# Optimization experiments

Hardware: AMD Instinct MI355X
Metric: run time of the kernel (lower is better)

## Reference

```python
import jax, jax.numpy as jnp
import numpy as np
import math

NUM_HEADS = 16
HEAD_DIM = 64
EMBED = NUM_HEADS * HEAD_DIM  # 1024
T_FEAT = 128


def setup_inputs() -> dict:
    key = jax.random.key(0)
    ks = jax.random.split(key, 9)
    B, S = 4, 2048
    x = jax.random.normal(ks[0], (B, S, EMBED), dtype=jnp.float32)
    time_enc = jax.random.normal(ks[1], (B, T_FEAT), dtype=jnp.float32)
    s = 1.0 / math.sqrt(EMBED)
    Wq = jax.random.normal(ks[2], (EMBED, EMBED), dtype=jnp.float32) * s
    Wk = jax.random.normal(ks[3], (EMBED, EMBED), dtype=jnp.float32) * s
    Wv = jax.random.normal(ks[4], (EMBED, EMBED), dtype=jnp.float32) * s
    Wo = jax.random.normal(ks[5], (EMBED, EMBED), dtype=jnp.float32) * s
    bo = jnp.zeros((EMBED,), dtype=jnp.float32)
    Wt = jax.random.normal(ks[6], (T_FEAT, NUM_HEADS), dtype=jnp.float32) * (1.0 / math.sqrt(T_FEAT))
    bt = jnp.zeros((NUM_HEADS,), dtype=jnp.float32)
    return {"x": x, "time_enc": time_enc, "Wq": Wq, "Wk": Wk, "Wv": Wv,
            "Wo": Wo, "bo": bo, "Wt": Wt, "bt": bt}


def reference(x, time_enc, Wq, Wk, Wv, Wo, bo, Wt, bt):
    B, S, E = x.shape
    H, D = NUM_HEADS, HEAD_DIM
    scale = 1.0 / math.sqrt(D)
    # projections (no bias on q/k/v, bias on out)
    q = (x @ Wq).reshape(B, S, H, D).transpose(0, 2, 1, 3)  # [B,H,S,D]
    k = (x @ Wk).reshape(B, S, H, D).transpose(0, 2, 1, 3)
    v = (x @ Wv).reshape(B, S, H, D).transpose(0, 2, 1, 3)
    scores = jnp.einsum('bhqd,bhkd->bhqk', q, k) * scale
    # time-dependent per-head weighting (softmax over heads)
    time_weights = jax.nn.softmax(time_enc @ Wt + bt)  # [B,H]
    scores = scores * time_weights.reshape(B, H, 1, 1)
    attn = jax.nn.softmax(scores, axis=-1)
    out = jnp.einsum('bhqk,bhkd->bhqd', attn, v)
    out = out.transpose(0, 2, 1, 3).reshape(B, S, E)
    return out @ Wo + bo
```

## Files before the change

kernel.cpp:

```cpp
#include <hip/hip_runtime.h>
#include <cstdint>
#include <cstddef>

#define EMB   1024
#define NH    16
#define HD    64
#define SEQ   2048
#define NB    4
#define MROWS 8192

typedef short short8 __attribute__((ext_vector_type(8)));
typedef float floatx4 __attribute__((ext_vector_type(4)));

__device__ __forceinline__ unsigned short f2bf(float f) {
  return (unsigned short)((__float_as_uint(f) + 0x8000u) >> 16);
}

__device__ __forceinline__ void load16_lds(const unsigned short* g, unsigned short* l) {
  __builtin_amdgcn_global_load_lds((const __attribute__((address_space(1))) void*)g,
                                   (__attribute__((address_space(3))) void*)l, 16, 0, 0);
}

__global__ void time_weights_kernel(const float* __restrict__ te, const float* __restrict__ Wt,
                                    const float* __restrict__ bt, float* __restrict__ tw) {
  int t = threadIdx.x;
  int b = t >> 4, h = t & 15;
  float acc = bt[h];
  for (int i = 0; i < 128; i++) acc += te[b * 128 + i] * Wt[i * 16 + h];
  float m = acc;
  for (int off = 1; off < 16; off <<= 1) m = fmaxf(m, __shfl_xor(m, off, 16));
  float e = __expf(acc - m);
  float s = e;
  for (int off = 1; off < 16; off <<= 1) s += __shfl_xor(s, off, 16);
  tw[t] = (e / s) * 0.125f * 1.4426950408889634f;
}

__global__ void convert_x_kernel(const float4* __restrict__ x, unsigned short* __restrict__ out) {
  int i = blockIdx.x * blockDim.x + threadIdx.x;
  float4 v = x[i];
  unsigned int u0 = __float_as_uint(v.x) + 0x8000u, u1 = __float_as_uint(v.y) + 0x8000u;
  unsigned int u2 = __float_as_uint(v.z) + 0x8000u, u3 = __float_as_uint(v.w) + 0x8000u;
  uint2 p;
  p.x = (u0 >> 16) | (u1 & 0xffff0000u);
  p.y = (u2 >> 16) | (u3 & 0xffff0000u);
  *(uint2*)&out[(size_t)i * 4] = p;
}

__global__ void transpose_convert4_kernel(const float* __restrict__ Wq, const float* __restrict__ Wk,
                                          const float* __restrict__ Wv, const float* __restrict__ Wo,
                                          unsigned short* __restrict__ wqkvt, unsigned short* __restrict__ wot) {
  __shared__ float tile[32][33];
  int z = blockIdx.z;
  const float* W = (z == 0) ? Wq : (z == 1) ? Wk : (z == 2) ? Wv : Wo;
  unsigned short* out = (z < 3) ? (wqkvt + (size_t)z * EMB * EMB) : wot;
  int k0 = blockIdx.x * 32;
  int n0 = blockIdx.y * 32;
  int tx = threadIdx.x;
  int ty = threadIdx.y;
#pragma unroll
  for (int i = 0; i < 4; i++) {
    int k = ty + i * 8;
    tile[k][tx] = W[(size_t)(k0 + k) * EMB + n0 + tx];
  }
  __syncthreads();
#pragma unroll
  for (int i = 0; i < 4; i++) {
    int n = ty + i * 8;
    out[(size_t)(n0 + n) * EMB + k0 + tx] = f2bf(tile[tx][n]);
  }
}

template <int EPI>
__global__ __launch_bounds__(256) void gemm_kernel(
    const unsigned short* __restrict__ A, const unsigned short* __restrict__ Bt,
    unsigned short* __restrict__ qo, unsigned short* __restrict__ ko, unsigned short* __restrict__ vto,
    float* __restrict__ outf, const float* __restrict__ bias, const float* __restrict__ tw) {
  __shared__ unsigned short As[128 * 64];
  __shared__ unsigned short Bs[128 * 64];

  int tid = threadIdx.x;
  int lane = tid & 63, wid = tid >> 6;
  int quad = lane >> 4, l16 = lane & 15;
  int wm = wid >> 1, wn = wid & 1;
  int m0 = blockIdx.y * 128, n0 = blockIdx.x * 128;

  const unsigned short* gA[4];
  const unsigned short* gB[4];
  unsigned short* lA[4];
  unsigned short* lB[4];
#pragma unroll
  for (int c = 0; c < 4; c++) {
    int row = wid * 32 + c * 8 + (lane >> 3);
    int gcol = ((lane & 7) ^ (row & 7)) * 8;
    gA[c] = A + (size_t)(m0 + row) * 1024 + gcol;
    gB[c] = Bt + (size_t)(n0 + row) * 1024 + gcol;
    lA[c] = &As[(wid * 32 + c * 8) * 64];
    lB[c] = &Bs[(wid * 32 + c * 8) * 64];
  }

  int aoff[2];
#pragma unroll
  for (int kk = 0; kk < 2; kk++) aoff[kk] = (((kk * 4 + quad) ^ (l16 & 7)) * 8);

  floatx4 acc[4][4];
#pragma unroll
  for (int mi = 0; mi < 4; mi++)
#pragma unroll
    for (int ni = 0; ni < 4; ni++)
#pragma unroll
      for (int r = 0; r < 4; r++) acc[mi][ni][r] = 0.f;

  for (int k0 = 0; k0 < 1024; k0 += 64) {
    __syncthreads();
#pragma unroll
    for (int c = 0; c < 4; c++) {
      load16_lds(gA[c] + k0, lA[c]);
      load16_lds(gB[c] + k0, lB[c]);
    }
    asm volatile("s_waitcnt vmcnt(0) lgkmcnt(0)" ::: "memory");
    __syncthreads();

#pragma unroll
    for (int kk = 0; kk < 2; kk++) {
      short8 a_frag[4], b_frag[4];
#pragma unroll
      for (int mi = 0; mi < 4; mi++)
        a_frag[mi] = *(const short8*)&As[(wm * 64 + mi * 16 + l16) * 64 + aoff[kk]];
#pragma unroll
      for (int ni = 0; ni < 4; ni++)
        b_frag[ni] = *(const short8*)&Bs[(wn * 64 + ni * 16 + l16) * 64 + aoff[kk]];
#pragma unroll
      for (int mi = 0; mi < 4; mi++)
#pragma unroll
        for (int ni = 0; ni < 4; ni++)
          acc[mi][ni] = __builtin_amdgcn_mfma_f32_16x16x32_bf16(a_frag[mi], b_frag[ni], acc[mi][ni], 0, 0, 0);
    }
  }

#pragma unroll
  for (int mi = 0; mi < 4; mi++)
#pragma unroll
    for (int ni = 0; ni < 4; ni++)
#pragma unroll
      for (int r = 0; r < 4; r++) {
        int m = m0 + wm * 64 + mi * 16 + quad * 4 + r;
        int n = n0 + wn * 64 + ni * 16 + l16;
        float val = acc[mi][ni][r];
        if (EPI == 0) {
          int b = m >> 11, s = m & 2047;
          int proj = n >> 10, rem = n & 1023, hh = rem >> 6, d = rem & 63;
          size_t bh = (size_t)(b * NH + hh);
          if (proj == 0)      qo[(bh * SEQ + s) * HD + d] = f2bf(val * tw[bh]);
          else if (proj == 1) ko[(bh * SEQ + s) * HD + d] = f2bf(val);
          else                vto[(bh * HD + d) * SEQ + s] = f2bf(val);
        } else {
          outf[(size_t)m * EMB + n] = val + bias[n];
        }
      }
}

__global__ __launch_bounds__(256, 4) void attn_kernel(
    const unsigned short* __restrict__ qg, const unsigned short* __restrict__ kg,
    const unsigned short* __restrict__ vtg, unsigned short* __restrict__ aog) {
  __shared__ unsigned short Ks[64 * 64];
  __shared__ unsigned short Vs[64 * 64];
  __shared__ unsigned short Ps[4 * 2048];

  int tid = threadIdx.x;
  int lane = tid & 63, wid = tid >> 6;
  int quad = lane >> 4, l16 = lane & 15, l7 = lane & 7;
  int qt = blockIdx.x, h = blockIdx.y, b = blockIdx.z;
  int bh = b * NH + h;
  const unsigned short* qbase = qg + (size_t)bh * SEQ * HD + (size_t)qt * 128 * HD;
  const unsigned short* kbase = kg + (size_t)bh * SEQ * HD;
  const unsigned short* vbase = vtg + (size_t)bh * HD * SEQ;

  short8 b_q[2][2];
#pragma unroll
  for (int mi = 0; mi < 2; mi++)
#pragma unroll
    for (int kk = 0; kk < 2; kk++)
      b_q[mi][kk] = *(const short8*)&qbase[(wid * 32 + mi * 16 + l16) * 64 + kk * 32 + quad * 8];

  const unsigned short* gK[2];
  const unsigned short* gV[2];
  unsigned short* lK[2];
  unsigned short* lV[2];
#pragma unroll
  for (int c = 0; c < 2; c++) {
    int row = wid * 16 + c * 8 + (lane >> 3);
    int gcol = ((lane & 7) ^ (row & 7)) * 8;
    gK[c] = kbase + row * 64 + gcol;
    gV[c] = vbase + (size_t)row * SEQ + gcol;
    lK[c] = &Ks[(wid * 16 + c * 8) * 64];
    lV[c] = &Vs[(wid * 16 + c * 8) * 64];
  }

  int pg[2];
#pragma unroll
  for (int i = 0; i < 2; i++) pg[i] = l16 * 64 + (((i * 4 + quad) ^ l7) * 8);

  int wbase = wid * 2048;
  int chunkx = l16 & 14;
  int pwa[4];
#pragma unroll
  for (int ni = 0; ni < 4; ni++)
    pwa[ni] = wbase + l16 * 64 + (((ni * 4 + quad) ^ chunkx) * 4);
  int pra[2];
#pragma unroll
  for (int kk2 = 0; kk2 < 2; kk2++)
    pra[kk2] = wbase + l16 * 64 + (((kk2 * 8 + quad * 2) ^ chunkx) * 4);

  floatx4 O[4][2];
  float lsum[2] = {0.f, 0.f};
#pragma unroll
  for (int di = 0; di < 4; di++)
#pragma unroll
    for (int mi = 0; mi < 2; mi++)
#pragma unroll
      for (int r = 0; r < 4; r++) O[di][mi][r] = 0.f;

  for (int kb = 0; kb < 32; kb++) {
    __syncthreads();
#pragma unroll
    for (int c = 0; c < 2; c++) {
      load16_lds(gK[c] + kb * 4096, lK[c]);
      load16_lds(gV[c] + kb * 64, lV[c]);
    }
    asm volatile("s_waitcnt vmcnt(0) lgkmcnt(0)" ::: "memory");
    __syncthreads();

    floatx4 st[4][2];
#pragma unroll
    for (int ni = 0; ni < 4; ni++)
#pragma unroll
      for (int mi = 0; mi < 2; mi++)
#pragma unroll
        for (int r = 0; r < 4; r++) st[ni][mi][r] = 0.f;
#pragma unroll
    for (int kk = 0; kk < 2; kk++)
#pragma unroll
      for (int ni = 0; ni < 4; ni++) {
        short8 a_k = *(const short8*)&Ks[ni * 1024 + pg[kk]];
#pragma unroll
        for (int mi = 0; mi < 2; mi++)
          st[ni][mi] = __builtin_amdgcn_mfma_f32_16x16x32_bf16(a_k, b_q[mi][kk], st[ni][mi], 0, 0, 0);
      }

#pragma unroll
    for (int mi = 0; mi < 2; mi++)
#pragma unroll
      for (int ni = 0; ni < 4; ni++) {
        float p0 = __builtin_amdgcn_exp2f(st[ni][mi][0]);
        float p1 = __builtin_amdgcn_exp2f(st[ni][mi][1]);
        float p2 = __builtin_amdgcn_exp2f(st[ni][mi][2]);
        float p3 = __builtin_amdgcn_exp2f(st[ni][mi][3]);
        lsum[mi] += (p0 + p1) + (p2 + p3);
        unsigned int u0 = __float_as_uint(p0) + 0x8000u, u1 = __float_as_uint(p1) + 0x8000u;
        unsigned int u2 = __float_as_uint(p2) + 0x8000u, u3 = __float_as_uint(p3) + 0x8000u;
        uint2 w;
        w.x = (u0 >> 16) | (u1 & 0xffff0000u);
        w.y = (u2 >> 16) | (u3 & 0xffff0000u);
        *(uint2*)&Ps[pwa[ni] + mi * 1024] = w;
      }
    asm volatile("s_waitcnt lgkmcnt(0)" ::: "memory");

#pragma unroll
    for (int kk2 = 0; kk2 < 2; kk2++) {
      short8 av[4], bp[2];
#pragma unroll
      for (int di = 0; di < 4; di++)
        av[di] = *(const short8*)&Vs[di * 1024 + pg[kk2]];
#pragma unroll
      for (int mi = 0; mi < 2; mi++)
        bp[mi] = *(const short8*)&Ps[pra[kk2] + mi * 1024];
#pragma unroll
      for (int di = 0; di < 4; di++)
#pragma unroll
        for (int mi = 0; mi < 2; mi++)
          O[di][mi] = __builtin_amdgcn_mfma_f32_16x16x32_bf16(av[di], bp[mi], O[di][mi], 0, 0, 0);
    }
  }

  float inv[2];
#pragma unroll
  for (int mi = 0; mi < 2; mi++) {
    lsum[mi] += __shfl_xor(lsum[mi], 16);
    lsum[mi] += __shfl_xor(lsum[mi], 32);
    inv[mi] = 1.0f / lsum[mi];
  }

#pragma unroll
  for (int mi = 0; mi < 2; mi++) {
    int s = qt * 128 + wid * 32 + mi * 16 + l16;
    size_t rowbase = ((size_t)(b * SEQ + s) * NH + h) * HD;
#pragma unroll
    for (int di = 0; di < 4; di++) {
      unsigned int u0 = __float_as_uint(O[di][mi][0] * inv[mi]) + 0x8000u;
      unsigned int u1 = __float_as_uint(O[di][mi][1] * inv[mi]) + 0x8000u;
      unsigned int u2 = __float_as_uint(O[di][mi][2] * inv[mi]) + 0x8000u;
      unsigned int u3 = __float_as_uint(O[di][mi][3] * inv[mi]) + 0x8000u;
      uint2 w;
      w.x = (u0 >> 16) | (u1 & 0xffff0000u);
      w.y = (u2 >> 16) | (u3 & 0xffff0000u);
      *(uint2*)&aog[rowbase + di * 16 + quad * 4] = w;
    }
  }
}

extern "C" void kernel_launch(void* const* d_in, const int* in_sizes, int n_in,
                              void* d_out, int out_size, void* d_ws, size_t ws_size,
                              hipStream_t stream) {
  (void)in_sizes; (void)n_in; (void)out_size; (void)ws_size;
  const float* x  = (const float*)d_in[0];
  const float* te = (const float*)d_in[1];
  const float* Wq = (const float*)d_in[2];
  const float* Wk = (const float*)d_in[3];
  const float* Wv = (const float*)d_in[4];
  const float* Wo = (const float*)d_in[5];
  const float* bo = (const float*)d_in[6];
  const float* Wt = (const float*)d_in[7];
  const float* bt = (const float*)d_in[8];
  float* out = (float*)d_out;

  char* ws = (char*)d_ws;
  size_t off = 0;
  auto carve = [&](size_t bytes) -> void* {
    void* p = ws + off;
    off += (bytes + 255) & ~(size_t)255;
    return p;
  };
  float* twb            = (float*)carve(64 * sizeof(float));
  unsigned short* xb    = (unsigned short*)carve((size_t)MROWS * EMB * 2);
  unsigned short* wqkvt = (unsigned short*)carve((size_t)3 * EMB * EMB * 2);
  unsigned short* wot   = (unsigned short*)carve((size_t)EMB * EMB * 2);
  unsigned short* vtb   = (unsigned short*)carve((size_t)MROWS * EMB * 2);
  unsigned short* qb    = (unsigned short*)d_out;
  unsigned short* kb    = (unsigned short*)d_out + (size_t)MROWS * EMB;
  unsigned short* ao    = xb;

  time_weights_kernel<<<dim3(1), dim3(64), 0, stream>>>(te, Wt, bt, twb);
  convert_x_kernel<<<dim3(8192), dim3(256), 0, stream>>>((const float4*)x, xb);
  transpose_convert4_kernel<<<dim3(32, 32, 4), dim3(32, 8), 0, stream>>>(Wq, Wk, Wv, Wo, wqkvt, wot);
  gemm_kernel<0><<<dim3(24, 64), dim3(256), 0, stream>>>(xb, wqkvt, qb, kb, vtb, nullptr, nullptr, twb);
  attn_kernel<<<dim3(16, NH, NB), dim3(256), 0, stream>>>(qb, kb, vtb, ao);
  gemm_kernel<1><<<dim3(8, 64), dim3(256), 0, stream>>>(ao, wot, nullptr, nullptr, nullptr, out, bo, nullptr);
}
```

Baseline: 324.6 us.

## Remap block indices for XCD-aware locality and shrink out-projection M tile

Flattens the GEMM and attention grids to 1D and remaps block IDs so that consecutive blocks (round-robined across the 8 XCDs) share B tiles or the same head's K/V. This is meant to improve L2 reuse per XCD. The output projection GEMM now uses a 64-row M tile, doubling its block count to 1024 for better occupancy and wave balance, at the cost of less A/B reuse per block. The swizzle column is simplified to use lane>>3, which matches the old row&7.

```diff
diff --git a/kernel.cpp b/kernel.cpp
--- a/kernel.cpp
+++ b/kernel.cpp
@@ -70,41 +70,61 @@
   }
 }
 
-template <int EPI>
+template <int EPI, int MT>
 __global__ __launch_bounds__(256) void gemm_kernel(
     const unsigned short* __restrict__ A, const unsigned short* __restrict__ Bt,
     unsigned short* __restrict__ qo, unsigned short* __restrict__ ko, unsigned short* __restrict__ vto,
     float* __restrict__ outf, const float* __restrict__ bias, const float* __restrict__ tw) {
-  __shared__ unsigned short As[128 * 64];
+  constexpr int MI = MT / 32;
+  constexpr int CA = MT / 32;
+  __shared__ unsigned short As[MT * 64];
   __shared__ unsigned short Bs[128 * 64];
 
   int tid = threadIdx.x;
   int lane = tid & 63, wid = tid >> 6;
   int quad = lane >> 4, l16 = lane & 15;
   int wm = wid >> 1, wn = wid & 1;
-  int m0 = blockIdx.y * 128, n0 = blockIdx.x * 128;
-
-  const unsigned short* gA[4];
+
+  int id = blockIdx.x;
+  int nt, mt;
+  if (EPI == 0) {
+    int x = id & 7;
+    unsigned int local = (unsigned int)id >> 3;
+    nt = x * 3 + (int)(local % 3u);
+    mt = (int)(local / 3u);
+  } else {
+    nt = id & 7;
+    mt = id >> 3;
+  }
+  int m0 = mt * MT, n0 = nt * 128;
+
+  const unsigned short* gA[CA];
+  unsigned short* lA[CA];
   const unsigned short* gB[4];
-  unsigned short* lA[4];
   unsigned short* lB[4];
-#pragma unroll
-  for (int c = 0; c < 4; c++) {
-    int row = wid * 32 + c * 8 + (lane >> 3);
-    int gcol = ((lane & 7) ^ (row & 7)) * 8;
-    gA[c] = A + (size_t)(m0 + row) * 1024 + gcol;
-    gB[c] = Bt + (size_t)(n0 + row) * 1024 + gcol;
-    lA[c] = &As[(wid * 32 + c * 8) * 64];
-    lB[c] = &Bs[(wid * 32 + c * 8) * 64];
+  {
+    int gcol = ((lane & 7) ^ (lane >> 3)) * 8;
+#pragma unroll
+    for (int c = 0; c < CA; c++) {
+      int row = wid * (MT / 4) + c * 8 + (lane >> 3);
+      gA[c] = A + (size_t)(m0 + row) * 1024 + gcol;
+      lA[c] = &As[(wid * (MT / 4) + c * 8) * 64];
+    }
+#pragma unroll
+    for (int c = 0; c < 4; c++) {
+      int row = wid * 32 + c * 8 + (lane >> 3);
+      gB[c] = Bt + (size_t)(n0 + row) * 1024 + gcol;
+      lB[c] = &Bs[(wid * 32 + c * 8) * 64];
+    }
   }
 
   int aoff[2];
 #pragma unroll
   for (int kk = 0; kk < 2; kk++) aoff[kk] = (((kk * 4 + quad) ^ (l16 & 7)) * 8);
 
-  floatx4 acc[4][4];
-#pragma unroll
-  for (int mi = 0; mi < 4; mi++)
+  floatx4 acc[MI][4];
+#pragma unroll
+  for (int mi = 0; mi < MI; mi++)
 #pragma unroll
     for (int ni = 0; ni < 4; ni++)
 #pragma unroll
@@ -113,24 +133,23 @@
   for (int k0 = 0; k0 < 1024; k0 += 64) {
     __syncthreads();
 #pragma unroll
-    for (int c = 0; c < 4; c++) {
-      load16_lds(gA[c] + k0, lA[c]);
-      load16_lds(gB[c] + k0, lB[c]);
-    }
+    for (int c = 0; c < CA; c++) load16_lds(gA[c] + k0, lA[c]);
+#pragma unroll
+    for (int c = 0; c < 4; c++) load16_lds(gB[c] + k0, lB[c]);
     asm volatile("s_waitcnt vmcnt(0) lgkmcnt(0)" ::: "memory");
     __syncthreads();
 
 #pragma unroll
     for (int kk = 0; kk < 2; kk++) {
-      short8 a_frag[4], b_frag[4];
-#pragma unroll
-      for (int mi = 0; mi < 4; mi++)
-        a_frag[mi] = *(const short8*)&As[(wm * 64 + mi * 16 + l16) * 64 + aoff[kk]];
+      short8 a_frag[MI], b_frag[4];
+#pragma unroll
+      for (int mi = 0; mi < MI; mi++)
+        a_frag[mi] = *(const short8*)&As[(wm * (MI * 16) + mi * 16 + l16) * 64 + aoff[kk]];
 #pragma unroll
       for (int ni = 0; ni < 4; ni++)
         b_frag[ni] = *(const short8*)&Bs[(wn * 64 + ni * 16 + l16) * 64 + aoff[kk]];
 #pragma unroll
-      for (int mi = 0; mi < 4; mi++)
+      for (int mi = 0; mi < MI; mi++)
 #pragma unroll
         for (int ni = 0; ni < 4; ni++)
           acc[mi][ni] = __builtin_amdgcn_mfma_f32_16x16x32_bf16(a_frag[mi], b_frag[ni], acc[mi][ni], 0, 0, 0);
@@ -138,12 +157,12 @@
   }
 
 #pragma unroll
-  for (int mi = 0; mi < 4; mi++)
+  for (int mi = 0; mi < MI; mi++)
 #pragma unroll
     for (int ni = 0; ni < 4; ni++)
 #pragma unroll
       for (int r = 0; r < 4; r++) {
-        int m = m0 + wm * 64 + mi * 16 + quad * 4 + r;
+        int m = m0 + wm * (MI * 16) + mi * 16 + quad * 4 + r;
         int n = n0 + wn * 64 + ni * 16 + l16;
         float val = acc[mi][ni][r];
         if (EPI == 0) {
@@ -169,8 +188,13 @@
   int tid = threadIdx.x;
   int lane = tid & 63, wid = tid >> 6;
   int quad = lane >> 4, l16 = lane & 15, l7 = lane & 7;
-  int qt = blockIdx.x, h = blockIdx.y, b = blockIdx.z;
-  int bh = b * NH + h;
+
+  int id = blockIdx.x;
+  int local = id >> 3;
+  int bh = (id & 7) * 8 + (local >> 4);
+  int qt = local & 15;
+  int b = bh >> 4, h = bh & 15;
+
   const unsigned short* qbase = qg + (size_t)bh * SEQ * HD + (size_t)qt * 128 * HD;
   const unsigned short* kbase = kg + (size_t)bh * SEQ * HD;
   const unsigned short* vbase = vtg + (size_t)bh * HD * SEQ;
@@ -342,7 +366,7 @@
   time_weights_kernel<<<dim3(1), dim3(64), 0, stream>>>(te, Wt, bt, twb);
   convert_x_kernel<<<dim3(8192), dim3(256), 0, stream>>>((const float4*)x, xb);
   transpose_convert4_kernel<<<dim3(32, 32, 4), dim3(32, 8), 0, stream>>>(Wq, Wk, Wv, Wo, wqkvt, wot);
-  gemm_kernel<0><<<dim3(24, 64), dim3(256), 0, stream>>>(xb, wqkvt, qb, kb, vtb, nullptr, nullptr, twb);
-  attn_kernel<<<dim3(16, NH, NB), dim3(256), 0, stream>>>(qb, kb, vtb, ao);
-  gemm_kernel<1><<<dim3(8, 64), dim3(256), 0, stream>>>(ao, wot, nullptr, nullptr, nullptr, out, bo, nullptr);
-}
+  gemm_kernel<0, 128><<<dim3(1536), dim3(256), 0, stream>>>(xb, wqkvt, qb, kb, vtb, nullptr, nullptr, twb);
+  attn_kernel<<<dim3(1024), dim3(256), 0, stream>>>(qb, kb, vtb, ao);
+  gemm_kernel<1, 64><<<dim3(1024), dim3(256), 0, stream>>>(ao, wot, nullptr, nullptr, nullptr, out, bo, nullptr);
+}
```

Result: no change. 325.0 us (+0.1%).
